# Kernel optimization log

Measured on AMD Instinct MI355X. Metric: run time of the kernel, lower is better.

The kernel has to match this reference:

```python
import jax, jax.numpy as jnp
import numpy as np

IN_CH, OUT_CH, K = 32, 32, 3

def setup_inputs() -> dict:
    key = jax.random.key(0)
    kx, kw = jax.random.split(key)
    x = jax.random.normal(kx, (16, IN_CH, 256, 256), dtype=jnp.float32)
    # weight matches nn.Parameter shape (out_channels, in_channels, k, k)
    weight = jax.random.normal(kw, (OUT_CH, IN_CH, K, K), dtype=jnp.float32) * 0.05
    return {"x": x, "weight": weight}

def reference(x, weight):
    # Valid (no-padding), stride-1 cross-correlation, identical math to the
    # per-pixel slice*weight sum in the torch module.
    return jax.lax.conv_general_dilated(
        x, weight,
        window_strides=(1, 1),
        padding='VALID',
        dimension_numbers=('NCHW', 'OIHW', 'NCHW'),
    )
```

## Files before the change

kernel.cpp:

```cpp
#include <hip/hip_runtime.h>
#include <hip/hip_bf16.h>


typedef __attribute__((ext_vector_type(8))) short bf16x8;
typedef __attribute__((ext_vector_type(4))) float f32x4;

#define MFMA(a,b,c) __builtin_amdgcn_mfma_f32_16x16x32_bf16((a),(b),(c),0,0,0)
#define SCHED0 __builtin_amdgcn_sched_barrier(0)
#define LGKMBAR asm volatile("s_waitcnt lgkmcnt(0)\n\ts_barrier" ::: "memory")

__device__ __forceinline__ unsigned short f2bf(float f) {
    unsigned int u = __float_as_uint(f);
    return (unsigned short)((u + 0x7FFFu + ((u >> 16) & 1u)) >> 16);
}
__device__ __forceinline__ unsigned int packpair(float a, float b) {
    __hip_bfloat162 t = __float22bfloat162_rn(make_float2(a, b));
    union { __hip_bfloat162 h; unsigned int u; } c;
    c.h = t;
    return c.u;
}

#define ROWW 132
#define SLOTW (16 * ROWW)

#define ROWCL(R_) ((R0 + (R_)) > 255 ? 255 : (R0 + (R_)))

#define ISSUE(R_) do {                                                       \
    const float* rp_ = xim + ((size_t)ROWCL(R_) << 8) + gpx;                 \
    gA[(R_) % 3] = *(const float4*)(rp_ + ((size_t)pA << 16));               \
    gB[(R_) % 3] = *(const float4*)(rp_ + (((size_t)pA + 1) << 16));         \
    if (h == 0 && wv == ((R_) & 7))                                          \
        gH[(R_) % 3] = *(const float2*)(xim + ((size_t)(lane >> 1) << 16)    \
                        + ((size_t)ROWCL(R_) << 8) + 128 + 2 * (lane & 1));  \
} while (0)

#define CVTW(R_) do {                                                        \
    const float4 A_ = gA[(R_) % 3], B_ = gB[(R_) % 3];                       \
    unsigned int* d_ = &L[((R_) & 7) * SLOTW + (2 * wv + lhi) * ROWW + 4 * l31]; \
    *(uint4*)d_ = make_uint4(packpair(A_.x, B_.x), packpair(A_.y, B_.y),     \
                             packpair(A_.z, B_.z), packpair(A_.w, B_.w));    \
    if (h == 0 && wv == ((R_) & 7)) {                                        \
        const float2 V_ = gH[(R_) % 3];                                      \
        unsigned short* hp_ = (unsigned short*)&L[((R_) & 7) * SLOTW         \
                              + (lane >> 2) * ROWW + 128 + 2 * (lane & 1)]   \
                              + ((lane >> 1) & 1);                           \
        hp_[0] = f2bf(V_.x); hp_[2] = f2bf(V_.y);                            \
    }                                                                        \
} while (0)

#define MROW(P_, KY_) do {                                                   \
    if ((P_) - (KY_) >= 0 && (P_) - (KY_) <= 15) {                           \
        acc[(P_)-(KY_)][0] = MFMA(a0_.v, wf[(KY_)*3+0][0], acc[(P_)-(KY_)][0]); \
        acc[(P_)-(KY_)][0] = MFMA(a1_.v, wf[(KY_)*3+1][0], acc[(P_)-(KY_)][0]); \
        acc[(P_)-(KY_)][0] = MFMA(a2_.v, wf[(KY_)*3+2][0], acc[(P_)-(KY_)][0]); \
        acc[(P_)-(KY_)][1] = MFMA(a0_.v, wf[(KY_)*3+0][1], acc[(P_)-(KY_)][1]); \
        acc[(P_)-(KY_)][1] = MFMA(a1_.v, wf[(KY_)*3+1][1], acc[(P_)-(KY_)][1]); \
        acc[(P_)-(KY_)][1] = MFMA(a2_.v, wf[(KY_)*3+2][1], acc[(P_)-(KY_)][1]); \
    }                                                                        \
} while (0)

#define COMP(P_) do {                                                        \
    union { unsigned int u[4]; bf16x8 v; } a0_, a1_, a2_;                    \
    const unsigned int* sb_ = &L[((P_) & 7) * SLOTW + (g << 2) * ROWW        \
                                 + (wv << 4) + l15];                         \
    a0_.u[0] = sb_[0*ROWW+0]; a1_.u[0] = sb_[0*ROWW+1]; a2_.u[0] = sb_[0*ROWW+2]; \
    a0_.u[1] = sb_[1*ROWW+0]; a1_.u[1] = sb_[1*ROWW+1]; a2_.u[1] = sb_[1*ROWW+2]; \
    a0_.u[2] = sb_[2*ROWW+0]; a1_.u[2] = sb_[2*ROWW+1]; a2_.u[2] = sb_[2*ROWW+2]; \
    a0_.u[3] = sb_[3*ROWW+0]; a1_.u[3] = sb_[3*ROWW+1]; a2_.u[3] = sb_[3*ROWW+2]; \
    MROW(P_, 0); MROW(P_, 1); MROW(P_, 2);                                   \
} while (0)

#define STORE(R_) do {                                                       \
    if ((R_) >= 0 && (R_) <= 15) {                                           \
        const int y_ = R0 + (R_);                                            \
        if (y_ < 254) {                                                      \
            const int xo_ = (h << 7) + (wv << 4) + (g << 2);                 \
            _Pragma("unroll")                                                \
            for (int hh_ = 0; hh_ < 2; ++hh_) {                              \
                const f32x4 v_ = acc[R_][hh_];                               \
                float* p_ = out + (size_t)((n << 5) | (hh_ << 4) | l15) * 64516 \
                          + y_ * 254 + xo_;                                  \
                if (xo_ + 3 < 254) {                                         \
                    *(float2*)p_       = make_float2(v_[0], v_[1]);          \
                    *(float2*)(p_ + 2) = make_float2(v_[2], v_[3]);          \
                } else if (xo_ + 1 < 254) {         \
                    *(float2*)p_ = make_float2(v_[0], v_[1]);                \
                }                                                            \
            }                                                                \
        }                                                                    \
    }                                                                        \
} while (0)

#define STEP2(P_) do {                                                       \
    LGKMBAR;                                                                 \
    COMP(P_);                                                                \
    COMP((P_) + 1);                                                          \
    STORE((P_) - 2);                                                         \
    STORE((P_) - 1);                                                         \
    SCHED0;                                                                  \
    if ((P_) + 2 <= 17) CVTW((P_) + 2);                                      \
    if ((P_) + 3 <= 17) CVTW((P_) + 3);                                      \
    SCHED0;                                                                  \
    if ((P_) + 4 <= 17) ISSUE((P_) + 4);                                     \
    if ((P_) + 5 <= 17) ISSUE((P_) + 5);                                     \
} while (0)

__global__ __launch_bounds__(512, 2)
void fconv(const float* __restrict__ x, const float* __restrict__ w,
           float* __restrict__ out) {
    __shared__ unsigned int L[8 * SLOTW];

    const int tid  = threadIdx.x;
    const int bid  = blockIdx.x;
    const int o    = ((bid & 7) << 6) | (bid >> 3);
    const int n    = o >> 5;
    const int rb   = (o >> 1) & 15;
    const int h    = o & 1;
    const int wv   = tid >> 6;
    const int lane = tid & 63;
    const int l15  = lane & 15;
    const int g    = lane >> 4;
    const int l31  = lane & 31;
    const int lhi  = lane >> 5;
    const int R0   = rb << 4;

    #pragma unroll
    for (int k = 0; k < 18; ++k)
        ((float*)L)[tid + (k << 9)] = w[tid + (k << 9)];
    __syncthreads();
    bf16x8 wf[9][2];
    {
        const float* wl = (const float*)L;
        #pragma unroll
        for (int tap = 0; tap < 9; ++tap)
            #pragma unroll
            for (int hh = 0; hh < 2; ++hh) {
                union { unsigned short s[8]; bf16x8 v; } u;
                #pragma unroll
                for (int e = 0; e < 8; ++e)
                    u.s[e] = f2bf(wl[(hh * 16 + l15) * 288 + (8 * g + e) * 9 + tap]);
                wf[tap][hh] = u.v;
            }
    }
    __syncthreads();

    if (h == 1) {
        const int s_ = tid >> 6, r_ = (tid >> 2) & 15, c_ = tid & 3;
        L[s_ * SLOTW + r_ * ROWW + 128 + c_] = 0u;
    }

    const float* xim = x + ((size_t)n << 21);
    const int    pA  = 4 * wv + 2 * lhi;
    const int    gpx = (h << 7) + 4 * l31;

    float4 gA[3], gB[3];
    float2 gH[3];

    f32x4 acc[16][2];
    #pragma unroll
    for (int r = 0; r < 16; ++r)
        #pragma unroll
        for (int hh = 0; hh < 2; ++hh) {
            f32x4 z = {0.f, 0.f, 0.f, 0.f};
            acc[r][hh] = z;
        }

    ISSUE(0); ISSUE(1); ISSUE(2);
    SCHED0;
    CVTW(0);
    ISSUE(3);
    CVTW(1);

    STEP2(0);  STEP2(2);  STEP2(4);  STEP2(6);  STEP2(8);
    STEP2(10); STEP2(12); STEP2(14); STEP2(16);
}

extern "C" void kernel_launch(void* const* d_in, const int* in_sizes, int n_in,
                              void* d_out, int out_size, void* d_ws, size_t ws_size,
                              hipStream_t stream) {
    const float* x = (const float*)d_in[0];
    const float* w = (const float*)d_in[1];
    float* out     = (float*)d_out;
    hipLaunchKernelGGL(fconv, dim3(512), dim3(512), 0, stream, x, w, out);
}
```

Before: 56.32 us.

## Stage conv outputs through LDS for coalesced row-contiguous global stores

Result: slower. 57.87 us (+2.8%).

```diff
diff --git a/kernel.cpp b/kernel.cpp
--- a/kernel.cpp
+++ b/kernel.cpp
@@ -22,6 +22,8 @@
 
 #define ROWW 132
 #define SLOTW (16 * ROWW)
+#define LOUT0 (8 * SLOTW)
+#define LOUTROW (32 * ROWW)
 
 #define ROWCL(R_) ((R0 + (R_)) > 255 ? 255 : (R0 + (R_)))
 
@@ -70,22 +72,29 @@
     MROW(P_, 0); MROW(P_, 1); MROW(P_, 2);                                   \
 } while (0)
 
-#define STORE(R_) do {                                                       \
+#define OUTW(R_) do {                                                        \
+    if ((R_) >= 0 && (R_) <= 15) {                                           \
+        _Pragma("unroll")                                                    \
+        for (int hh_ = 0; hh_ < 2; ++hh_) {                                  \
+            const int co_ = (hh_ << 4) | l15;                                \
+            float* dw_ = (float*)&L[LOUT0 + ((R_) & 1) * LOUTROW             \
+                                    + co_ * ROWW + (wv << 4) + (g << 2)];    \
+            *(f32x4*)dw_ = acc[R_][hh_];                                     \
+        }                                                                    \
+    }                                                                        \
+} while (0)
+
+#define OUTRD(R_) do {                                                       \
     if ((R_) >= 0 && (R_) <= 15) {                                           \
         const int y_ = R0 + (R_);                                            \
-        if (y_ < 254) {                                                      \
-            const int xo_ = (h << 7) + (wv << 4) + (g << 2);                 \
+        if (y_ < 254 && (h == 0 || lane < 63)) {                             \
             _Pragma("unroll")                                                \
-            for (int hh_ = 0; hh_ < 2; ++hh_) {                              \
-                const f32x4 v_ = acc[R_][hh_];                               \
-                float* p_ = out + (size_t)((n << 5) | (hh_ << 4) | l15) * 64516 \
-                          + y_ * 254 + xo_;                                  \
-                if (xo_ + 3 < 254) {                                         \
-                    *(float2*)p_       = make_float2(v_[0], v_[1]);          \
-                    *(float2*)(p_ + 2) = make_float2(v_[2], v_[3]);          \
-                } else if (xo_ + 1 < 254) {         \
-                    *(float2*)p_ = make_float2(v_[0], v_[1]);                \
-                }                                                            \
+            for (int k_ = 0; k_ < 4; ++k_) {                                 \
+                const int co_ = (wv << 2) | k_;                              \
+                const float2 v_ = *(const float2*)&L[LOUT0 + ((R_) & 1) * LOUTROW \
+                                                     + co_ * ROWW + 2 * lane];    \
+                *(float2*)(out + (size_t)((n << 5) | co_) * 64516            \
+                           + y_ * 254 + (h << 7) + 2 * lane) = v_;           \
             }                                                                \
         }                                                                    \
     }                                                                        \
@@ -95,20 +104,23 @@
     LGKMBAR;                                                                 \
     COMP(P_);                                                                \
     COMP((P_) + 1);                                                          \
-    STORE((P_) - 2);                                                         \
-    STORE((P_) - 1);                                                         \
+    OUTW((P_) - 2);                                                          \
+    OUTW((P_) - 1);                                                          \
     SCHED0;                                                                  \
     if ((P_) + 2 <= 17) CVTW((P_) + 2);                                      \
     if ((P_) + 3 <= 17) CVTW((P_) + 3);                                      \
     SCHED0;                                                                  \
     if ((P_) + 4 <= 17) ISSUE((P_) + 4);                                     \
     if ((P_) + 5 <= 17) ISSUE((P_) + 5);                                     \
+    LGKMBAR;                                                                 \
+    OUTRD((P_) - 2);                                                         \
+    OUTRD((P_) - 1);                                                         \
 } while (0)
 
-__global__ __launch_bounds__(512, 2)
+__global__ __launch_bounds__(512, 1)
 void fconv(const float* __restrict__ x, const float* __restrict__ w,
            float* __restrict__ out) {
-    __shared__ unsigned int L[8 * SLOTW];
+    __shared__ unsigned int L[8 * SLOTW + 2 * LOUTROW];
 
     const int tid  = threadIdx.x;
     const int bid  = blockIdx.x;
```
